# Performance work log

Hardware: AMD Instinct MI355X
Metric: run time of the kernel (lower is better)

The kernel has to match this reference:

```python
import jax, jax.numpy as jnp
import numpy as np

NUM_EXPERTS = 8
HIDDEN = 1024
INTER = 2816
T = 16          # tokens
TOP_K = 2       # active experts per token
INIT_STD = 0.02


def setup_inputs() -> dict:
    key = jax.random.key(0)
    k_x, k_idx, k_g, k_u, k_d = jax.random.split(key, 5)
    x = jax.random.normal(k_x, (T, HIDDEN), dtype=jnp.float32)
    expert_indices = jax.random.randint(k_idx, (T, TOP_K), 0, NUM_EXPERTS)
    gate_proj = INIT_STD * jax.random.normal(k_g, (NUM_EXPERTS, INTER, HIDDEN), dtype=jnp.float32)
    up_proj = INIT_STD * jax.random.normal(k_u, (NUM_EXPERTS, HIDDEN, INTER), dtype=jnp.float32)
    down_proj = INIT_STD * jax.random.normal(k_d, (NUM_EXPERTS, INTER, HIDDEN), dtype=jnp.float32)
    return {"x": x, "expert_indices": expert_indices,
            "gate_proj": gate_proj, "up_proj": up_proj, "down_proj": down_proj}


def reference(x, expert_indices, gate_proj, up_proj, down_proj):
    # Faithful to the torch module, including its swapped proj naming:
    #   gate branch: gate_proj[idx] : [t, a, I, H]
    #   'down' branch (acts as up): down_proj[idx] : [t, a, I, H]
    #   final contraction: up_proj[idx] : [t, a, H, I]
    gw = gate_proj[expert_indices]          # [t, a, I, H]
    dw = down_proj[expert_indices]          # [t, a, I, H]
    uw = up_proj[expert_indices]            # [t, a, H, I]
    x1 = jax.nn.silu(jnp.einsum('ti,taoi->tao', x, gw))  # [t, a, I]
    x3 = jnp.einsum('ti,taoi->tao', x, dw)               # [t, a, I]
    expert_outs = jnp.einsum('tao,taio->tai', x1 * x3, uw)  # [t, a, H]
    return expert_outs
```

## Files before the change

kernel.cpp:

```cpp
#include <hip/hip_runtime.h>

#define NE 8
#define HD 1024
#define IW 2816
#define NT 16
#define TK 2
#define NP (NT*TK)
#define NPC1 8
#define NPC2 8

__global__ __launch_bounds__(256) void moe_phase1(
    const float* __restrict__ x,
    const int*   __restrict__ idx,
    const float* __restrict__ gate,
    const float* __restrict__ down,
    float*       __restrict__ hbuf)
{
    __shared__ int s_list[NP];
    __shared__ int s_n;
    const int e = blockIdx.y;
    {
        const int t = threadIdx.x;
        const bool mine = (t < NP) && (idx[t] == e);
        const unsigned long long m = __ballot(mine);
        if (mine) s_list[__popcll(m & ((1ull << t) - 1ull))] = t;
        if (t == 0) s_n = (int)__popcll(m);
    }
    __syncthreads();
    const int npl = s_n;
    if (npl == 0) return;

    const int wave = threadIdx.x >> 6;
    const int lane = threadIdx.x & 63;
    const int o = blockIdx.x * 4 + wave;

    const float* grow = gate + ((size_t)e * IW + o) * HD + lane * 4;
    const float* drow = down + ((size_t)e * IW + o) * HD + lane * 4;
    float gw[16], dw[16];
    #pragma unroll
    for (int c = 0; c < 4; ++c) {
        float4 gv = *(const float4*)(grow + c * 256);
        float4 dv = *(const float4*)(drow + c * 256);
        gw[4*c+0]=gv.x; gw[4*c+1]=gv.y; gw[4*c+2]=gv.z; gw[4*c+3]=gv.w;
        dw[4*c+0]=dv.x; dw[4*c+1]=dv.y; dw[4*c+2]=dv.z; dw[4*c+3]=dv.w;
    }

    for (int n0 = 0; n0 < npl; n0 += NPC1) {
        const int nc = (npl - n0 < NPC1) ? (npl - n0) : NPC1;
        float ag[NPC1], ad[NPC1];
        #pragma unroll
        for (int j = 0; j < NPC1; ++j) {
            ag[j] = 0.f; ad[j] = 0.f;
            if (j < nc) {
                const float* xrow = x + (size_t)(s_list[n0 + j] >> 1) * HD + lane * 4;
                #pragma unroll
                for (int c = 0; c < 4; ++c) {
                    float4 xv = *(const float4*)(xrow + c * 256);
                    ag[j] += xv.x*gw[4*c+0] + xv.y*gw[4*c+1] + xv.z*gw[4*c+2] + xv.w*gw[4*c+3];
                    ad[j] += xv.x*dw[4*c+0] + xv.y*dw[4*c+1] + xv.z*dw[4*c+2] + xv.w*dw[4*c+3];
                }
            }
        }
        #pragma unroll
        for (int off = 32; off > 0; off >>= 1) {
            #pragma unroll
            for (int j = 0; j < NPC1; ++j) {
                if (j < nc) {
                    ag[j] += __shfl_xor(ag[j], off, 64);
                    ad[j] += __shfl_xor(ad[j], off, 64);
                }
            }
        }
        if (lane == 0) {
            #pragma unroll
            for (int j = 0; j < NPC1; ++j) {
                if (j < nc) {
                    const float g = ag[j];
                    const float s = g / (1.f + __expf(-g));
                    hbuf[(size_t)s_list[n0 + j] * IW + o] = s * ad[j];
                }
            }
        }
    }
}

__global__ __launch_bounds__(256) void moe_phase2(
    const float* __restrict__ up,
    const int*   __restrict__ idx,
    const float* __restrict__ hbuf,
    float*       __restrict__ out)
{
    __shared__ int s_list[NP];
    __shared__ int s_n;
    const int e = blockIdx.y;
    {
        const int t = threadIdx.x;
        const bool mine = (t < NP) && (idx[t] == e);
        const unsigned long long m = __ballot(mine);
        if (mine) s_list[__popcll(m & ((1ull << t) - 1ull))] = t;
        if (t == 0) s_n = (int)__popcll(m);
    }
    __syncthreads();
    const int npl = s_n;
    if (npl == 0) return;

    const int wave = threadIdx.x >> 6;
    const int lane = threadIdx.x & 63;
    const int h = blockIdx.x * 4 + wave;

    const float* urow = up + ((size_t)e * HD + h) * IW + lane * 4;
    float w[44];
    #pragma unroll
    for (int c = 0; c < 11; ++c) {
        float4 uv = *(const float4*)(urow + c * 256);
        w[4*c+0]=uv.x; w[4*c+1]=uv.y; w[4*c+2]=uv.z; w[4*c+3]=uv.w;
    }

    for (int n0 = 0; n0 < npl; n0 += NPC2) {
        const int nc = (npl - n0 < NPC2) ? (npl - n0) : NPC2;
        float acc[NPC2];
        #pragma unroll
        for (int j = 0; j < NPC2; ++j) {
            acc[j] = 0.f;
            if (j < nc) {
                const float* hrow = hbuf + (size_t)s_list[n0 + j] * IW + lane * 4;
                #pragma unroll
                for (int c = 0; c < 11; ++c) {
                    float4 hv = *(const float4*)(hrow + c * 256);
                    acc[j] += w[4*c+0]*hv.x + w[4*c+1]*hv.y + w[4*c+2]*hv.z + w[4*c+3]*hv.w;
                }
            }
        }
        #pragma unroll
        for (int off = 32; off > 0; off >>= 1) {
            #pragma unroll
            for (int j = 0; j < NPC2; ++j) {
                if (j < nc) acc[j] += __shfl_xor(acc[j], off, 64);
            }
        }
        if (lane == 0) {
            #pragma unroll
            for (int j = 0; j < NPC2; ++j) {
                if (j < nc) out[(size_t)s_list[n0 + j] * HD + h] = acc[j];
            }
        }
    }
}

extern "C" void kernel_launch(void* const* d_in, const int* in_sizes, int n_in,
                              void* d_out, int out_size, void* d_ws, size_t ws_size,
                              hipStream_t stream) {
    const float* x    = (const float*)d_in[0];
    const int*   idx  = (const int*)  d_in[1];
    const float* gate = (const float*)d_in[2];
    const float* up   = (const float*)d_in[3];
    const float* down = (const float*)d_in[4];
    float* hbuf = (float*)d_ws;
    float* out  = (float*)d_out;

    moe_phase1<<<dim3(IW/4, NE), dim3(256), 0, stream>>>(x, idx, gate, down, hbuf);
    moe_phase2<<<dim3(HD/4, NE), dim3(256), 0, stream>>>(up, idx, hbuf, out);
}
```

Measured before the change: 276.7 us.

## Stage token activations in LDS and split waves across multiple weight rows

Phase 1 now loads up to eight selected token rows of x into shared memory once per block. Each wave handles four output rows, with 16 lanes per row, and streams the gate/down weights directly instead of preloading them into registers. Phase 2 assigns two rows per wave (32 lanes each) and streams the up weights with fixed-count unrolled loops. This aims to reuse x across rows, cut redundant global x loads and shorten the shuffle reductions, at the cost of extra shared memory, barriers and wasted work on padded token slots.

```diff
diff --git a/kernel.cpp b/kernel.cpp
--- a/kernel.cpp
+++ b/kernel.cpp
@@ -6,8 +6,7 @@
 #define NT 16
 #define TK 2
 #define NP (NT*TK)
-#define NPC1 8
-#define NPC2 8
+#define NPC 8
 
 __global__ __launch_bounds__(256) void moe_phase1(
     const float* __restrict__ x,
@@ -16,6 +15,7 @@
     const float* __restrict__ down,
     float*       __restrict__ hbuf)
 {
+    __shared__ float s_x[NPC][HD];
     __shared__ int s_list[NP];
     __shared__ int s_n;
     const int e = blockIdx.y;
@@ -32,52 +32,60 @@
 
     const int wave = threadIdx.x >> 6;
     const int lane = threadIdx.x & 63;
-    const int o = blockIdx.x * 4 + wave;
+    const int rloc = lane >> 4;
+    const int kg   = lane & 15;
+    const int orow = blockIdx.x * 16 + wave * 4 + rloc;
 
-    const float* grow = gate + ((size_t)e * IW + o) * HD + lane * 4;
-    const float* drow = down + ((size_t)e * IW + o) * HD + lane * 4;
-    float gw[16], dw[16];
-    #pragma unroll
-    for (int c = 0; c < 4; ++c) {
-        float4 gv = *(const float4*)(grow + c * 256);
-        float4 dv = *(const float4*)(drow + c * 256);
-        gw[4*c+0]=gv.x; gw[4*c+1]=gv.y; gw[4*c+2]=gv.z; gw[4*c+3]=gv.w;
-        dw[4*c+0]=dv.x; dw[4*c+1]=dv.y; dw[4*c+2]=dv.z; dw[4*c+3]=dv.w;
-    }
+    const float* gp = gate + ((size_t)e * IW + orow) * HD + kg * 4;
+    const float* dp = down + ((size_t)e * IW + orow) * HD + kg * 4;
 
-    for (int n0 = 0; n0 < npl; n0 += NPC1) {
-        const int nc = (npl - n0 < NPC1) ? (npl - n0) : NPC1;
-        float ag[NPC1], ad[NPC1];
-        #pragma unroll
-        for (int j = 0; j < NPC1; ++j) {
-            ag[j] = 0.f; ad[j] = 0.f;
-            if (j < nc) {
-                const float* xrow = x + (size_t)(s_list[n0 + j] >> 1) * HD + lane * 4;
-                #pragma unroll
-                for (int c = 0; c < 4; ++c) {
-                    float4 xv = *(const float4*)(xrow + c * 256);
-                    ag[j] += xv.x*gw[4*c+0] + xv.y*gw[4*c+1] + xv.z*gw[4*c+2] + xv.w*gw[4*c+3];
-                    ad[j] += xv.x*dw[4*c+0] + xv.y*dw[4*c+1] + xv.z*dw[4*c+2] + xv.w*dw[4*c+3];
+    for (int g0 = 0; g0 < npl; g0 += NPC) {
+        const int nc = (npl - g0 < NPC) ? (npl - g0) : NPC;
+        __syncthreads();
+        {
+            const int t = threadIdx.x;
+            #pragma unroll
+            for (int j = 0; j < NPC; ++j) {
+                if (j < nc) {
+                    const int tok = s_list[g0 + j] >> 1;
+                    *(float4*)&s_x[j][t * 4] = *(const float4*)(x + (size_t)tok * HD + t * 4);
+                } else {
+                    *(float4*)&s_x[j][t * 4] = make_float4(0.f, 0.f, 0.f, 0.f);
                 }
             }
         }
+        __syncthreads();
+
+        float ag[NPC], ad[NPC];
         #pragma unroll
-        for (int off = 32; off > 0; off >>= 1) {
+        for (int j = 0; j < NPC; ++j) { ag[j] = 0.f; ad[j] = 0.f; }
+
+        #pragma unroll 4
+        for (int s = 0; s < 16; ++s) {
+            const float4 g4 = *(const float4*)(gp + s * 64);
+            const float4 d4 = *(const float4*)(dp + s * 64);
             #pragma unroll
-            for (int j = 0; j < NPC1; ++j) {
-                if (j < nc) {
-                    ag[j] += __shfl_xor(ag[j], off, 64);
-                    ad[j] += __shfl_xor(ad[j], off, 64);
-                }
+            for (int j = 0; j < NPC; ++j) {
+                const float4 x4 = *(const float4*)&s_x[j][s * 64 + kg * 4];
+                ag[j] += g4.x*x4.x + g4.y*x4.y + g4.z*x4.z + g4.w*x4.w;
+                ad[j] += d4.x*x4.x + d4.y*x4.y + d4.z*x4.z + d4.w*x4.w;
             }
         }
-        if (lane == 0) {
+        #pragma unroll
+        for (int off = 1; off < 16; off <<= 1) {
             #pragma unroll
-            for (int j = 0; j < NPC1; ++j) {
+            for (int j = 0; j < NPC; ++j) {
+                ag[j] += __shfl_xor(ag[j], off, 64);
+                ad[j] += __shfl_xor(ad[j], off, 64);
+            }
+        }
+        if (kg == 0) {
+            #pragma unroll
+            for (int j = 0; j < NPC; ++j) {
                 if (j < nc) {
                     const float g = ag[j];
-                    const float s = g / (1.f + __expf(-g));
-                    hbuf[(size_t)s_list[n0 + j] * IW + o] = s * ad[j];
+                    const float sg = g / (1.f + __expf(-g));
+                    hbuf[(size_t)s_list[g0 + j] * IW + orow] = sg * ad[j];
                 }
             }
         }
@@ -106,43 +114,44 @@
 
     const int wave = threadIdx.x >> 6;
     const int lane = threadIdx.x & 63;
-    const int h = blockIdx.x * 4 + wave;
+    const int rloc = lane >> 5;
+    const int kg   = lane & 31;
+    const int hrow = blockIdx.x * 8 + wave * 2 + rloc;
 
-    const float* urow = up + ((size_t)e * HD + h) * IW + lane * 4;
-    float w[44];
-    #pragma unroll
-    for (int c = 0; c < 11; ++c) {
-        float4 uv = *(const float4*)(urow + c * 256);
-        w[4*c+0]=uv.x; w[4*c+1]=uv.y; w[4*c+2]=uv.z; w[4*c+3]=uv.w;
-    }
+    const float* upp = up + ((size_t)e * HD + hrow) * IW + kg * 4;
 
-    for (int n0 = 0; n0 < npl; n0 += NPC2) {
-        const int nc = (npl - n0 < NPC2) ? (npl - n0) : NPC2;
-        float acc[NPC2];
+    for (int g0 = 0; g0 < npl; g0 += NPC) {
+        const int nc = (npl - g0 < NPC) ? (npl - g0) : NPC;
+        const float* hp[NPC];
         #pragma unroll
-        for (int j = 0; j < NPC2; ++j) {
-            acc[j] = 0.f;
-            if (j < nc) {
-                const float* hrow = hbuf + (size_t)s_list[n0 + j] * IW + lane * 4;
-                #pragma unroll
-                for (int c = 0; c < 11; ++c) {
-                    float4 hv = *(const float4*)(hrow + c * 256);
-                    acc[j] += w[4*c+0]*hv.x + w[4*c+1]*hv.y + w[4*c+2]*hv.z + w[4*c+3]*hv.w;
-                }
+        for (int j = 0; j < NPC; ++j) {
+            const int p = s_list[g0 + (j < nc ? j : 0)];
+            hp[j] = hbuf + (size_t)p * IW + kg * 4;
+        }
+
+        float acc[NPC];
+        #pragma unroll
+        for (int j = 0; j < NPC; ++j) acc[j] = 0.f;
+
+        #pragma unroll 2
+        for (int s = 0; s < 22; ++s) {
+            const float4 u4 = *(const float4*)(upp + s * 128);
+            #pragma unroll
+            for (int j = 0; j < NPC; ++j) {
+                const float4 h4 = *(const float4*)(hp[j] + s * 128);
+                acc[j] += u4.x*h4.x + u4.y*h4.y + u4.z*h4.z + u4.w*h4.w;
             }
         }
         #pragma unroll
-        for (int off = 32; off > 0; off >>= 1) {
+        for (int off = 1; off < 32; off <<= 1) {
             #pragma unroll
-            for (int j = 0; j < NPC2; ++j) {
-                if (j < nc) acc[j] += __shfl_xor(acc[j], off, 64);
-            }
+            for (int j = 0; j < NPC; ++j)
+                acc[j] += __shfl_xor(acc[j], off, 64);
         }
-        if (lane == 0) {
+        if (kg == 0) {
             #pragma unroll
-            for (int j = 0; j < NPC2; ++j) {
-                if (j < nc) out[(size_t)s_list[n0 + j] * HD + h] = acc[j];
-            }
+            for (int j = 0; j < NPC; ++j)
+                if (j < nc) out[(size_t)s_list[g0 + j] * HD + hrow] = acc[j];
         }
     }
 }
@@ -158,6 +167,6 @@
     float* hbuf = (float*)d_ws;
     float* out  = (float*)d_out;
 
-    moe_phase1<<<dim3(IW/4, NE), dim3(256), 0, stream>>>(x, idx, gate, down, hbuf);
-    moe_phase2<<<dim3(HD/4, NE), dim3(256), 0, stream>>>(up, idx, hbuf, out);
+    moe_phase1<<<dim3(IW / 16, NE), dim3(256), 0, stream>>>(x, idx, gate, down, hbuf);
+    moe_phase2<<<dim3(HD / 8, NE), dim3(256), 0, stream>>>(up, idx, hbuf, out);
 }
```

Result: slower. 296.5 us (+7.1%).
